# Performance work log

Measured on AMD Instinct MI355X. Metric: run time of the kernel, lower is better.

Reference implementation:

```python
import jax, jax.numpy as jnp
import numpy as np

ROWS, COLS = 6, 7


def setup_inputs() -> dict:
    key = jax.random.key(0)
    k1, k2 = jax.random.split(key)
    N = 524288
    # gravity-consistent connect-4 boards: each column filled from the bottom
    heights = jax.random.randint(k1, (N, COLS), 0, ROWS + 1)          # pieces per column
    r = jnp.arange(ROWS)[None, :, None]                               # row 0 is top
    filled = r >= (ROWS - heights)[:, None, :]                        # (N, R, C)
    signs = jnp.where(jax.random.bernoulli(k2, 0.5, (N, ROWS, COLS)), 1.0, -1.0)
    x = jnp.where(filled, signs, 0.0).astype(jnp.float32)
    return {"x": x}


def _wins_and_playable(B):
    """For board B (N,R,C) from current player's (+1) perspective, return
    playable (N,C): column not full, and win (N,C): dropping +1 there wins."""
    N = B.shape[0]
    zero = B == 0
    playable = zero[:, 0, :]                                          # (N, C) top cell empty
    rows = jnp.arange(ROWS)
    # landing row = lowest (max-index) empty row per column; -1 if full (masked later)
    land = jnp.max(jnp.where(zero, rows[None, :, None], -1), axis=1)  # (N, C)
    n_idx = jnp.arange(N)[:, None]
    cols = jnp.arange(COLS)[None, :]
    win = jnp.zeros((N, COLS), dtype=bool)
    for dr, dc in ((0, 1), (1, 0), (1, 1), (1, -1)):
        cells = []
        for k in range(-3, 4):
            if k == 0:
                cells.append(jnp.ones((N, COLS), dtype=bool))         # the placed piece itself
                continue
            rr = land + k * dr                                        # (N, C)
            cc = cols + k * dc                                        # (1, C) -> broadcast
            valid = (rr >= 0) & (rr < ROWS) & (cc >= 0) & (cc < COLS)
            v = B[n_idx, jnp.clip(rr, 0, ROWS - 1), jnp.clip(cc, 0, COLS - 1)]
            cells.append(valid & (v == 1.0))
        cells = jnp.stack(cells, axis=-1)                             # (N, C, 7) offsets -3..3
        for s in range(4):                                            # any 4 consecutive
            win = win | jnp.all(cells[..., s:s + 4], axis=-1)
    return playable, win


def reference(x):
    squeeze = x.ndim == 2
    if squeeze:
        x = x[None]
    valids = []
    for sign in (1.0, -1.0):
        playable, win = _wins_and_playable(sign * x)
        valids.append(playable & win)
    valid = jnp.concatenate(valids, axis=1)                           # (N, 2C), priority order
    first = jnp.argmax(valid, axis=1)                                 # first True in scan order
    any_v = jnp.any(valid, axis=1)
    col = first % COLS
    logits = jnp.where(any_v[:, None],
                       jnp.log(jax.nn.one_hot(col, COLS, dtype=jnp.float32) + 1e-12),
                       0.0).astype(jnp.float32)
    return logits[0] if squeeze else logits
```

## Files before the change

kernel.cpp:

```cpp
#include <hip/hip_runtime.h>
#include <stdint.h>

#define ONE_BITS    0x3f800000u
#define NEGONE_BITS 0xbf800000u

#define THREADS 256
#define BOARDS_PER_BLOCK 256

static __device__ __forceinline__ uint64_t win_cells(uint64_t P) {
    uint64_t w = 0;
    #pragma unroll
    for (int d = 0; d < 4; ++d) {
        const int s = (d == 0) ? 1 : (d == 1) ? 7 : (d == 2) ? 8 : 9;
        uint64_t r1 = P >> s, r2 = P >> (2 * s), r3 = P >> (3 * s);
        uint64_t l1 = P << s, l2 = P << (2 * s), l3 = P << (3 * s);
        uint64_t a = r1 & r2;
        uint64_t b = l1 & l2;
        w |= (a & r3) | (a & l1) | (b & r1) | (b & l3);
    }
    return w;
}

static __device__ __forceinline__ uint32_t colfold(uint64_t v) {
    v |= v >> 8;
    v |= v >> 16;
    v |= v >> 32;
    return (uint32_t)v & 0x7Fu;
}

extern "C" __global__ void __launch_bounds__(256)
c4_kernel(const float* __restrict__ x, float* __restrict__ out)
{
    __shared__ float s_in[BOARDS_PER_BLOCK * 42];
    __shared__ float s_out[BOARDS_PER_BLOCK * 7];

    const int tid = threadIdx.x;
    const size_t board0 = (size_t)blockIdx.x * BOARDS_PER_BLOCK;

    const float2* src = reinterpret_cast<const float2*>(x) + board0 * 21u;
    float2* sin2 = reinterpret_cast<float2*>(s_in);
    #pragma unroll
    for (int k = 0; k < 21; ++k) {
        int n = k * THREADS + tid;
        sin2[n] = src[n];
    }
    __syncthreads();

    const float* my = s_in + tid * 42;
    uint32_t plo = 0, phi = 0, mlo = 0, mhi = 0;
    #pragma unroll
    for (int idx = 0; idx < 42; ++idx) {
        uint32_t u = __float_as_uint(my[idx]);
        const int sh = (idx / 7) * 8 + (idx % 7);
        uint32_t isP = (u == ONE_BITS)    ? 1u : 0u;
        uint32_t isM = (u == NEGONE_BITS) ? 1u : 0u;
        if (sh < 32) { plo |= isP << sh;        mlo |= isM << sh; }
        else         { phi |= isP << (sh - 32); mhi |= isM << (sh - 32); }
    }

    uint64_t P   = (uint64_t)plo | ((uint64_t)phi << 32);
    uint64_t M   = (uint64_t)mlo | ((uint64_t)mhi << 32);
    uint64_t occ = P | M;
    const uint64_t BOARD = 0x00007F7F7F7F7F7FULL;
    const uint64_t ROW5  = 0x00007F0000000000ULL;
    uint64_t land = ~occ & BOARD & ((occ >> 8) | ROW5);

    uint32_t cp = colfold(land & win_cells(P));
    uint32_t cm = colfold(land & win_cells(M));
    uint32_t sel = cp ? cp : cm;
    bool any = (sel != 0u);
    int col  = __ffs(sel) - 1;

    #pragma unroll
    for (int c = 0; c < 7; ++c)
        s_out[tid * 7 + c] = (any && c != col) ? -27.631021f : 0.0f;
    __syncthreads();

    float* dst = out + board0 * 7u;
    #pragma unroll
    for (int k = 0; k < 7; ++k) {
        int n = k * THREADS + tid;
        dst[n] = s_out[n];
    }
}

extern "C" void kernel_launch(void* const* d_in, const int* in_sizes, int n_in,
                              void* d_out, int out_size, void* d_ws, size_t ws_size,
                              hipStream_t stream)
{
    const float* x = (const float*)d_in[0];
    float* out = (float*)d_out;
    const int N = in_sizes[0] / 42;
    const int grid = N / BOARDS_PER_BLOCK;
    hipLaunchKernelGGL(c4_kernel, dim3(grid), dim3(THREADS), 0, stream, x, out);
}
```

Measured before the change: 21.77 us.

## Pack board floats into bytes in LDS and process two boards per thread

Loads input as float4 and compresses each float to its top byte via perm before storing to LDS, cutting LDS footprint and bank traffic by four. Each thread now handles two boards, extracting occupancy and opponent bits with multiply-based bit gathers and switching to a dense 7-bit-per-row bitboard with column masks guarding horizontal/diagonal wraparound. Block size doubles to 512 boards, which halves the grid and changes occupancy. It relies on values being exactly 0, +1 or -1, so sign and exponent bits identify cells.

```diff
diff --git a/kernel.cpp b/kernel.cpp
--- a/kernel.cpp
+++ b/kernel.cpp
@@ -1,84 +1,107 @@
 #include <hip/hip_runtime.h>
 #include <stdint.h>
 
-#define ONE_BITS    0x3f800000u
-#define NEGONE_BITS 0xbf800000u
+#define THREADS 256
+#define BOARDS_PER_BLOCK 512
 
-#define THREADS 256
-#define BOARDS_PER_BLOCK 256
+static constexpr uint64_t colmask(int lo, int hi) {
+    uint64_t m = 0;
+    for (int r = 0; r < 6; ++r)
+        for (int c = lo; c <= hi; ++c)
+            m |= 1ull << (7 * r + c);
+    return m;
+}
 
 static __device__ __forceinline__ uint64_t win_cells(uint64_t P) {
     uint64_t w = 0;
     #pragma unroll
     for (int d = 0; d < 4; ++d) {
-        const int s = (d == 0) ? 1 : (d == 1) ? 7 : (d == 2) ? 8 : 9;
+        const int s  = (d == 0) ? 1 : (d == 1) ? 7 : (d == 2) ? 8 : 6;
+        const int dc = (d == 0) ? 1 : (d == 1) ? 0 : (d == 2) ? 1 : -1;
+        const uint64_t M0 = (dc == 0) ? ~0ull : (dc > 0 ? colmask(0, 3) : colmask(3, 6));
+        const uint64_t M1 = (dc == 0) ? ~0ull : (dc > 0 ? colmask(1, 4) : colmask(2, 5));
+        const uint64_t M2 = (dc == 0) ? ~0ull : (dc > 0 ? colmask(2, 5) : colmask(1, 4));
+        const uint64_t M3 = (dc == 0) ? ~0ull : (dc > 0 ? colmask(3, 6) : colmask(0, 3));
         uint64_t r1 = P >> s, r2 = P >> (2 * s), r3 = P >> (3 * s);
         uint64_t l1 = P << s, l2 = P << (2 * s), l3 = P << (3 * s);
-        uint64_t a = r1 & r2;
-        uint64_t b = l1 & l2;
-        w |= (a & r3) | (a & l1) | (b & r1) | (b & l3);
+        uint64_t u = r1 & r2, v = l1 & l2;
+        w |= (u & r3 & M0) | (u & l1 & M1) | (v & r1 & M2) | (v & l3 & M3);
     }
     return w;
 }
 
 static __device__ __forceinline__ uint32_t colfold(uint64_t v) {
-    v |= v >> 8;
-    v |= v >> 16;
-    v |= v >> 32;
+    v |= v >> 21;
+    v |= v >> 7;
+    v |= v >> 7;
     return (uint32_t)v & 0x7Fu;
 }
 
-extern "C" __global__ void __launch_bounds__(256)
+extern "C" __global__ void __launch_bounds__(THREADS)
 c4_kernel(const float* __restrict__ x, float* __restrict__ out)
 {
-    __shared__ float s_in[BOARDS_PER_BLOCK * 42];
-    __shared__ float s_out[BOARDS_PER_BLOCK * 7];
+    __shared__ uint32_t s_pk[BOARDS_PER_BLOCK * 42 / 4];
+    __shared__ float    s_out[BOARDS_PER_BLOCK * 7];
 
     const int tid = threadIdx.x;
     const size_t board0 = (size_t)blockIdx.x * BOARDS_PER_BLOCK;
 
-    const float2* src = reinterpret_cast<const float2*>(x) + board0 * 21u;
-    float2* sin2 = reinterpret_cast<float2*>(s_in);
+    const float4* src = reinterpret_cast<const float4*>(x) + (size_t)blockIdx.x * 5376u;
     #pragma unroll
     for (int k = 0; k < 21; ++k) {
         int n = k * THREADS + tid;
-        sin2[n] = src[n];
+        float4 v = src[n];
+        uint32_t a = __float_as_uint(v.x), b = __float_as_uint(v.y),
+                 c = __float_as_uint(v.z), d = __float_as_uint(v.w);
+        uint32_t lo = __builtin_amdgcn_perm(b, a, 0x00000703u) & 0x0000FFFFu;
+        uint32_t hi = __builtin_amdgcn_perm(d, c, 0x07030000u) & 0xFFFF0000u;
+        s_pk[n] = lo | hi;
     }
     __syncthreads();
 
-    const float* my = s_in + tid * 42;
-    uint32_t plo = 0, phi = 0, mlo = 0, mhi = 0;
+    const uint32_t* pk = s_pk + tid * 21;
+    uint64_t occ[2] = {0, 0}, MM[2] = {0, 0};
     #pragma unroll
-    for (int idx = 0; idx < 42; ++idx) {
-        uint32_t u = __float_as_uint(my[idx]);
-        const int sh = (idx / 7) * 8 + (idx % 7);
-        uint32_t isP = (u == ONE_BITS)    ? 1u : 0u;
-        uint32_t isM = (u == NEGONE_BITS) ? 1u : 0u;
-        if (sh < 32) { plo |= isP << sh;        mlo |= isM << sh; }
-        else         { phi |= isP << (sh - 32); mhi |= isM << (sh - 32); }
+    for (int j = 0; j < 21; ++j) {
+        uint32_t e = pk[j];
+        uint32_t nO = ((e & 0x20202020u) * 0x00204081u) >> 26;
+        uint32_t nM = ((e & 0x80808080u) * 0x00204081u) >> 28;
+        if (j < 10) {
+            occ[0] |= (uint64_t)nO << (4 * j);
+            MM[0]  |= (uint64_t)nM << (4 * j);
+        } else if (j == 10) {
+            occ[0] |= (uint64_t)(nO & 3u) << 40;
+            MM[0]  |= (uint64_t)(nM & 3u) << 40;
+            occ[1] |= (uint64_t)(nO >> 2);
+            MM[1]  |= (uint64_t)(nM >> 2);
+        } else {
+            occ[1] |= (uint64_t)nO << (4 * j - 42);
+            MM[1]  |= (uint64_t)nM << (4 * j - 42);
+        }
     }
 
-    uint64_t P   = (uint64_t)plo | ((uint64_t)phi << 32);
-    uint64_t M   = (uint64_t)mlo | ((uint64_t)mhi << 32);
-    uint64_t occ = P | M;
-    const uint64_t BOARD = 0x00007F7F7F7F7F7FULL;
-    const uint64_t ROW5  = 0x00007F0000000000ULL;
-    uint64_t land = ~occ & BOARD & ((occ >> 8) | ROW5);
+    #pragma unroll
+    for (int b = 0; b < 2; ++b) {
+        uint64_t o = occ[b], m = MM[b], p = o & ~m;
+        const uint64_t ROW5 = 0x7Full << 35;
+        uint64_t land = ~o & ((o >> 7) | ROW5);
 
-    uint32_t cp = colfold(land & win_cells(P));
-    uint32_t cm = colfold(land & win_cells(M));
-    uint32_t sel = cp ? cp : cm;
-    bool any = (sel != 0u);
-    int col  = __ffs(sel) - 1;
+        uint32_t cp = colfold(land & win_cells(p));
+        uint32_t cm = colfold(land & win_cells(m));
+        uint32_t sel = cp ? cp : cm;
+        bool any = (sel != 0u);
+        int col  = __ffs(sel) - 1;
 
-    #pragma unroll
-    for (int c = 0; c < 7; ++c)
-        s_out[tid * 7 + c] = (any && c != col) ? -27.631021f : 0.0f;
+        float* so = s_out + (2 * tid + b) * 7;
+        #pragma unroll
+        for (int c = 0; c < 7; ++c)
+            so[c] = (any && c != col) ? -27.631021f : 0.0f;
+    }
     __syncthreads();
 
     float* dst = out + board0 * 7u;
     #pragma unroll
-    for (int k = 0; k < 7; ++k) {
+    for (int k = 0; k < 14; ++k) {
         int n = k * THREADS + tid;
         dst[n] = s_out[n];
     }
```

Result: no change. 21.55 us (-1.0%).
